# Optimization experiments

Measured on AMD Instinct MI355X. Metric: run time of the kernel, lower is better.

The kernel has to match this reference:

```python
import jax, jax.numpy as jnp
import numpy as np

EPS = 1e-6
NUM_HEADS = 12


def ln_cf(x, w, b):
    # channels_first LayerNorm over channel dim (ConvNeXt style)
    u = jnp.mean(x, axis=1, keepdims=True)
    s = jnp.mean((x - u) ** 2, axis=1, keepdims=True)
    xn = (x - u) / jnp.sqrt(s + EPS)
    shp = (1, -1) + (1,) * (x.ndim - 2)
    return xn * w.reshape(shp) + b.reshape(shp)


def conv2s2(x, w):
    # Conv3d kernel=2 stride=2 (no bias): exact non-overlapping patch contraction
    b, c, H, W, D = x.shape
    xp = x.reshape(b, c, H // 2, 2, W // 2, 2, D // 2, 2)
    return jnp.einsum('bchkwpdq,ockpq->bohwd', xp, w)


def convt2s2(x, w):
    # ConvTranspose3d kernel=2 stride=2 (torch weight layout [in, out, 2,2,2])
    b, i, H, W, D = x.shape
    o = w.shape[1]
    y = jnp.einsum('bihwd,iokpq->bohkwpdq', x, w)
    return y.reshape(b, o, 2 * H, 2 * W, 2 * D)


def stem(x, w1, g1, b1, w2, g2, b2):
    h = conv2s2(x, w1)
    h = jax.nn.gelu(ln_cf(h, g1, b1), approximate=False)
    h = conv2s2(h, w2)
    return ln_cf(h, g2, b2)


def debed(x, tw1, g, b, tw2, tb2):
    h = convt2s2(x, tw1)
    h = jax.nn.gelu(ln_cf(h, g, b), approximate=False)
    return convt2s2(h, tw2) + tb2.reshape(1, -1, 1, 1, 1)


def rope(x):
    # rotary embedding over full token dim c (pairs (i, i+c/2)), positions 0..L-1
    b, l, c = x.shape
    inv = 1.0 / (10000.0 ** (jnp.arange(0, c, 2, dtype=jnp.float32) / c))
    t = jnp.arange(l, dtype=jnp.float32)
    f = jnp.outer(t, inv)                      # [l, c/2]
    emb = jnp.concatenate([f, f], axis=-1)     # [l, c]
    cos, sin = jnp.cos(emb)[None], jnp.sin(emb)[None]
    rot = jnp.concatenate([-x[..., c // 2:], x[..., :c // 2]], axis=-1)
    return x * cos + rot * sin


def _forward(x, skip, q_w1, q_g1, q_b1, q_w2, q_g2, q_b2,
             k_w1, k_g1, k_b1, k_w2, k_g2, k_b2,
             v_w1, v_g1, v_b1, v_w2, v_g2, v_b2,
             o_tw1, o_g, o_b, o_tw2, o_tb2,
             ns_w, ns_b, nx_w, nx_b, no_w, no_b):
    res = skip
    skip = ln_cf(skip, ns_w, ns_b)
    x = ln_cf(x, nx_w, nx_b)
    q = stem(skip, q_w1, q_g1, q_b1, q_w2, q_g2, q_b2)
    k = stem(x, k_w1, k_g1, k_b1, k_w2, k_g2, k_b2)
    v = stem(x, v_w1, v_g1, v_b1, v_w2, v_g2, v_b2)
    b, c, Hq, Wq, Dq = q.shape
    _, _, Hk, Wk, Dk = k.shape
    q = q.reshape(b, c, -1).transpose(0, 2, 1)   # [b, Lq, c]
    k = k.reshape(b, c, -1).transpose(0, 2, 1)   # [b, Lk, c]
    v = v.reshape(b, c, -1).transpose(0, 2, 1)
    q = rope(q)
    k = rope(k)
    hd = c // NUM_HEADS
    qh = q.reshape(b, -1, NUM_HEADS, hd).transpose(0, 2, 1, 3)  # [b, nh, Lq, hd]
    kh = k.reshape(b, -1, NUM_HEADS, hd).transpose(0, 2, 1, 3)
    vh = v.reshape(b, -1, NUM_HEADS, hd).transpose(0, 2, 1, 3)
    scale = 1.0 / jnp.sqrt(jnp.float32(hd))
    attn = jax.nn.softmax(jnp.einsum('bhqc,bhkc->bhqk', qh, kh) * scale, axis=-1)
    proj = jnp.einsum('bhqk,bhkc->bhqc', attn, vh)              # [b, nh, Lq, hd]
    # rearrange 'b nh l c -> b (c nh) h w d'
    proj = proj.transpose(0, 3, 1, 2).reshape(b, c, Hq, Wq, Dq)
    proj = ln_cf(proj, no_w, no_b)
    out = debed(proj, o_tw1, o_g, o_b, o_tw2, o_tb2)
    return out + res


def setup_inputs() -> dict:
    key = jax.random.key(0)
    ks = iter(jax.random.split(key, 40))
    def nrm(shape, scale):
        return jax.random.normal(next(ks), shape, jnp.float32) * scale
    E, E4, XF, SF = 768, 192, 6, 6
    inp = {
        'x': nrm((2, XF, 48, 48, 48), 1.0),
        'skip': nrm((2, SF, 48, 48, 48), 1.0),
    }
    for p, ic in [('q', SF), ('k', XF), ('v', XF)]:
        inp[p + '_w1'] = nrm((E4, ic, 2, 2, 2), (ic * 8) ** -0.5)
        inp[p + '_g1'] = jnp.ones(E4, jnp.float32)
        inp[p + '_b1'] = jnp.zeros(E4, jnp.float32)
        inp[p + '_w2'] = nrm((E, E4, 2, 2, 2), (E4 * 8) ** -0.5)
        inp[p + '_g2'] = jnp.ones(E, jnp.float32)
        inp[p + '_b2'] = jnp.zeros(E, jnp.float32)
    inp['o_tw1'] = nrm((E, E4, 2, 2, 2), E ** -0.5)
    inp['o_g'] = jnp.ones(E4, jnp.float32)
    inp['o_b'] = jnp.zeros(E4, jnp.float32)
    inp['o_tw2'] = nrm((E4, SF, 2, 2, 2), E4 ** -0.5)
    inp['o_tb2'] = jnp.zeros(SF, jnp.float32)
    inp['ns_w'] = jnp.ones(SF, jnp.float32)
    inp['ns_b'] = jnp.zeros(SF, jnp.float32)
    inp['nx_w'] = jnp.ones(XF, jnp.float32)
    inp['nx_b'] = jnp.zeros(XF, jnp.float32)
    inp['no_w'] = jnp.ones(E, jnp.float32)
    inp['no_b'] = jnp.zeros(E, jnp.float32)
    return inp


def reference(x, skip, q_w1, q_g1, q_b1, q_w2, q_g2, q_b2,
              k_w1, k_g1, k_b1, k_w2, k_g2, k_b2,
              v_w1, v_g1, v_b1, v_w2, v_g2, v_b2,
              o_tw1, o_g, o_b, o_tw2, o_tb2,
              ns_w, ns_b, nx_w, nx_b, no_w, no_b):
    return _forward(x, skip, q_w1, q_g1, q_b1, q_w2, q_g2, q_b2,
                    k_w1, k_g1, k_b1, k_w2, k_g2, k_b2,
                    v_w1, v_g1, v_b1, v_w2, v_g2, v_b2,
                    o_tw1, o_g, o_b, o_tw2, o_tb2,
                    ns_w, ns_b, nx_w, nx_b, no_w, no_b)
```

## Files before the change

kernel.cpp:

```cpp
#include <hip/hip_runtime.h>
#include <math.h>

#define BB_ 2
#define C0 6
#define S0 48
#define V0 (S0*S0*S0)
#define C1 192
#define S1 24
#define V1 (S1*S1*S1)
#define C2 768
#define S2 12
#define LL (S2*S2*S2)
#define NH 12
#define HD 64
#define KDIM (C1*8)
#define MDIM (BB_*LL)

typedef __attribute__((ext_vector_type(8))) short short8;
typedef __attribute__((ext_vector_type(4))) short short4v;
typedef __attribute__((ext_vector_type(4))) float float4v;

static __device__ __forceinline__ float gelu_exact(float x){
  return 0.5f*x*(1.0f+erff(x*0.70710678118654752440f));
}
static __device__ __forceinline__ unsigned short f2bf(float f){
  unsigned int u = __float_as_uint(f);
  unsigned int r = (u + 0x7fffu + ((u>>16)&1u)) >> 16;
  return (unsigned short)r;
}
static __device__ __forceinline__ unsigned int pk_bf16(float a, float b){
#if __has_builtin(__builtin_amdgcn_cvt_pk_bf16_f32)
  typedef __attribute__((ext_vector_type(2))) __bf16 bf2;
  bf2 r = __builtin_amdgcn_cvt_pk_bf16_f32(a,b);
  union { bf2 v; unsigned int u; } cv; cv.v = r;
  return cv.u;
#else
  return (unsigned int)f2bf(a) | ((unsigned int)f2bf(b)<<16);
#endif
}
static __device__ __forceinline__ float bf2f(unsigned short u){
  return __uint_as_float(((unsigned int)u)<<16);
}
static __device__ __forceinline__ float exp2v(float x){
#if __has_builtin(__builtin_amdgcn_exp2f)
  return __builtin_amdgcn_exp2f(x);
#else
  return exp2f(x);
#endif
}
static __device__ __forceinline__ void load_lds16(const void* g, void* l){
  __builtin_amdgcn_global_load_lds((const __attribute__((address_space(1))) unsigned int*)g,
      (__attribute__((address_space(3))) unsigned int*)l, 16, 0, 0);
}
static __device__ __forceinline__ float4v mfma32(short8 a, short8 b, float4v c){
  return __builtin_amdgcn_mfma_f32_16x16x32_bf16(a,b,c,0,0,0);
}
static __device__ __forceinline__ float4v mfma16(short4v a, short4v b, float4v c){
#if __has_builtin(__builtin_amdgcn_mfma_f32_16x16x16bf16_1k)
  return __builtin_amdgcn_mfma_f32_16x16x16bf16_1k(a,b,c,0,0,0);
#else
  asm volatile("v_mfma_f32_16x16x16_bf16 %0, %1, %2, %0" : "+v"(c) : "v"(a), "v"(b));
  return c;
#endif
}

__global__ __launch_bounds__(256) void prep_kernel(
    const float* __restrict__ skin, const float* __restrict__ xin,
    const float* __restrict__ nsw, const float* __restrict__ nsb,
    const float* __restrict__ nxw, const float* __restrict__ nxb,
    unsigned short* __restrict__ outS, unsigned short* __restrict__ outX,
    const float* __restrict__ qw2, const float* __restrict__ kw2, const float* __restrict__ vw2,
    const float* __restrict__ tw1, const float* __restrict__ tw2,
    const float* __restrict__ qw1, const float* __restrict__ kw1, const float* __restrict__ vw1,
    unsigned short* __restrict__ w2tq, unsigned short* __restrict__ w2tk,
    unsigned short* __restrict__ w2tv, unsigned short* __restrict__ Btd,
    unsigned short* __restrict__ Bt48,
    unsigned short* __restrict__ w1q, unsigned short* __restrict__ w1k,
    unsigned short* __restrict__ w1v){
  int bx = blockIdx.x;
  if (bx < 1728){
    int z = bx >= 864;
    const float* in = z ? xin : skin;
    const float* w  = z ? nxw : nsw;
    const float* bi = z ? nxb : nsb;
    unsigned short* out = z ? outX : outS;
    int idx = (bx - z*864)*256 + threadIdx.x;
    int b = idx / V0, vox = idx - b*V0;
    const float* p = in + (size_t)b*(C0*V0) + vox;
    float v[C0]; float s=0.f;
#pragma unroll
    for (int c=0;c<C0;c++){ v[c]=p[(size_t)c*V0]; s+=v[c]; }
    float u = s*(1.f/C0);
    float ss=0.f;
#pragma unroll
    for (int c=0;c<C0;c++){ float d=v[c]-u; ss+=d*d; }
    float inv = rsqrtf(ss*(1.f/C0)+1e-6f);
    unsigned short* o = out + (size_t)b*(C0*V0) + vox;
#pragma unroll
    for (int c=0;c<C0;c++) o[(size_t)c*V0] = f2bf((v[c]-u)*inv*w[c]+bi[c]);
    return;
  }
  bx -= 1728;
  if (bx < 13824){
    int z = bx/4608;
    int idx = (bx - z*4608)*256 + threadIdx.x;
    const float* w2 = (z==0)?qw2:((z==1)?kw2:vw2);
    unsigned short* o = (z==0)?w2tq:((z==1)?w2tk:w2tv);
    int oc = idx/KDIM; int r = idx-oc*KDIM; int p = r/C1; int ic = r-p*C1;
    o[idx] = f2bf(w2[(size_t)oc*KDIM + ic*8 + p]);
  } else if (bx < 18432){
    int idx = (bx-13824)*256 + threadIdx.x;
    int n = idx/C2; int p = idx-n*C2;
    int i = ((p&63)*NH) + (p>>6);
    int kpq = n/C1, o2 = n-kpq*C1;
    Btd[idx] = f2bf(tw1[(size_t)i*KDIM + o2*8 + kpq]);
  } else if (bx < 18480){
    int idx = (bx-18432)*256 + threadIdx.x;
    int n = idx/C1; int i = idx-n*C1;
    Bt48[idx] = (n<48) ? f2bf(tw2[(size_t)i*48 + n]) : (unsigned short)0;
  } else {
    int idx = (bx-18480)*256 + threadIdx.x;
    int z = idx / 9216; int r = idx - z*9216;
    const float* w1 = (z==0)?qw1:((z==1)?kw1:vw1);
    unsigned short* o = (z==0)?w1q:((z==1)?w1k:w1v);
    o[r] = f2bf(w1[r]);
  }
}

__global__ __launch_bounds__(256) void conv1_kernel(
    const unsigned short* __restrict__ lnSb, const unsigned short* __restrict__ lnXb,
    const unsigned short* __restrict__ w1bq, const unsigned short* __restrict__ w1bk,
    const unsigned short* __restrict__ w1bv,
    const float* __restrict__ qg1, const float* __restrict__ qb1,
    const float* __restrict__ kg1, const float* __restrict__ kb1,
    const float* __restrict__ vg1, const float* __restrict__ vb1,
    unsigned short* __restrict__ h1q, unsigned short* __restrict__ h1k,
    unsigned short* __restrict__ h1v){
  int z = blockIdx.z;
  const unsigned short* in = (z==0)? lnSb : lnXb;
  const unsigned short* Wb = (z==0)?w1bq:((z==1)?w1bk:w1bv);
  const float* g1 = (z==0)?qg1:((z==1)?kg1:vg1);
  const float* b1 = (z==0)?qb1:((z==1)?kb1:vb1);
  unsigned short* h1p = (z==0)?h1q:((z==1)?h1k:h1v);
  int t = threadIdx.x, w = t>>6, lane = t&63;
  int g = lane>>4, l16 = lane&15;
  int j = blockIdx.x*4 + w;
  int bxh = j/18, mt = j - bxh*18;
  int b = bxh/48; int rem = bxh - b*48; int y = rem>>1, xh = rem&1;
  int xo = mt/3, zo = mt - xo*3;
  int xv = xh*12 + xo*2 + (l16>>3);
  int zv = zo*8 + (l16&7);
  int x2 = 2*xv, z2 = 2*zv, y2 = 2*y;
  const unsigned short* base = in + (size_t)b*C0*V0;
  union { short8 v; unsigned int u[4]; } aA;
  {
    size_t rb = (size_t)g*V0;
    aA.u[0] = *(const unsigned int*)&base[rb + (y2+0)*(S0*S0) + (x2+0)*S0 + z2];
    aA.u[1] = *(const unsigned int*)&base[rb + (y2+0)*(S0*S0) + (x2+1)*S0 + z2];
    aA.u[2] = *(const unsigned int*)&base[rb + (y2+1)*(S0*S0) + (x2+0)*S0 + z2];
    aA.u[3] = *(const unsigned int*)&base[rb + (y2+1)*(S0*S0) + (x2+1)*S0 + z2];
  }
  union { short4v v; unsigned int u[2]; } aB;
  {
    size_t rb = (size_t)(4+(g>>1))*V0 + (y2+(g&1))*(S0*S0);
    aB.u[0] = *(const unsigned int*)&base[rb + (x2+0)*S0 + z2];
    aB.u[1] = *(const unsigned int*)&base[rb + (x2+1)*S0 + z2];
  }
  float4v acc[12];
#pragma unroll
  for (int ot=0; ot<12; ot++){
    short8  wA = *(const short8*)&Wb[(ot*16+l16)*48 + g*8];
    short4v wB = *(const short4v*)&Wb[(ot*16+l16)*48 + 32 + g*4];
    float4v a = {};
    a = mfma32(wA, aA.v, a);
    a = mfma16(wB, aB.v, a);
    acc[ot] = a;
  }
  float s1=0.f, s2=0.f;
#pragma unroll
  for (int ot=0;ot<12;ot++)
#pragma unroll
    for (int reg=0;reg<4;reg++){ float v=acc[ot][reg]; s1+=v; s2+=v*v; }
  s1 += __shfl_xor(s1,16); s1 += __shfl_xor(s1,32);
  s2 += __shfl_xor(s2,16); s2 += __shfl_xor(s2,32);
  float u = s1*(1.f/C1);
  float inv = rsqrtf(s2*(1.f/C1)-u*u+1e-6f);
  int tok = (y>>1)*(S2*S2) + (xv>>1)*S2 + (zv>>1);
  int p8 = (y&1)*4 + (xv&1)*2 + (zv&1);
  unsigned short* hb = h1p + (size_t)(b*LL+tok)*KDIM + p8*C1;
#pragma unroll
  for (int ot=0; ot<12; ot++){
    int oc0 = ot*16 + g*4;
    float4 gg = *(const float4*)&g1[oc0];
    float4 bb = *(const float4*)&b1[oc0];
    float x0 = gelu_exact((acc[ot][0]-u)*inv*gg.x+bb.x);
    float x1 = gelu_exact((acc[ot][1]-u)*inv*gg.y+bb.y);
    float x2e= gelu_exact((acc[ot][2]-u)*inv*gg.z+bb.z);
    float x3 = gelu_exact((acc[ot][3]-u)*inv*gg.w+bb.w);
    uint2 pk; pk.x = pk_bf16(x0,x1); pk.y = pk_bf16(x2e,x3);
    *(uint2*)&hb[oc0] = pk;
  }
}

__global__ __launch_bounds__(256) void gemm_stem_kernel(
    const unsigned short* __restrict__ A0, const unsigned short* __restrict__ A1,
    const unsigned short* __restrict__ A2,
    const unsigned short* __restrict__ B0, const unsigned short* __restrict__ B1,
    const unsigned short* __restrict__ B2,
    unsigned short* __restrict__ Cq, unsigned short* __restrict__ Ck,
    unsigned short* __restrict__ Cv){
  int flat = blockIdx.x;
  int xcd = flat & 7, slot = flat >> 3;
  int tile = xcd*122 + slot;
  if (tile >= 972) return;
  int z = tile/324; int rr = tile - z*324;
  int m0 = (rr/12)*128, n0 = (rr - (rr/12)*12)*64;
  const unsigned short* A = (z==0)?A0:((z==1)?A1:A2);
  const unsigned short* Bt = (z==0)?B0:((z==1)?B1:B2);
  unsigned short* Cp = (z==0)?Cq:((z==1)?Ck:Cv);
  __shared__ __align__(16) unsigned short Al[3][128*32];
  __shared__ __align__(16) unsigned short Bl[3][64*32];
  int t=threadIdx.x, w=t>>6, lane=t&63;
  int g=lane>>4, l16=lane&15, r16=lane>>2, c16=lane&3;
  int wm=w>>1, wn=w&1;
  int csrc = (c16 ^ ((r16>>1)&3))*8;
  int crd  = (g   ^ ((l16>>1)&3))*8;
  float4v acc[4][2] = {};
  auto STAGE = [&](int buf, int kcol){
#pragma unroll
    for (int cc=0;cc<3;cc++){
      int ch = w*3+cc;
      if (ch<8) load_lds16(A + (size_t)(m0+ch*16+r16)*KDIM + kcol + csrc, &Al[buf][ch*512]);
      else      load_lds16(Bt + (size_t)(n0+(ch-8)*16+r16)*KDIM + kcol + csrc, &Bl[buf][(ch-8)*512]);
    }
  };
  auto COMPUTE = [&](int buf){
    short8 af[4], bf[2];
#pragma unroll
    for (int mt=0;mt<4;mt++) af[mt] = *(const short8*)&Al[buf][(wm*64+mt*16+l16)*32 + crd];
#pragma unroll
    for (int nt=0;nt<2;nt++) bf[nt] = *(const short8*)&Bl[buf][(wn*32+nt*16+l16)*32 + crd];
#pragma unroll
    for (int mt=0;mt<4;mt++)
#pragma unroll
      for (int nt=0;nt<2;nt++)
        acc[mt][nt] = mfma32(af[mt], bf[nt], acc[mt][nt]);
  };
  const int NT = KDIM/32;
  STAGE(0, 0);
  STAGE(1, 32);
  asm volatile("s_waitcnt vmcnt(3)" ::: "memory");
  __builtin_amdgcn_s_barrier();
  __builtin_amdgcn_sched_barrier(0);
  int cur = 0;
  for (int tt=0; tt<NT-2; tt++){
    int nb = cur+2; if (nb>=3) nb-=3;
    STAGE(nb, tt*32+64);
    COMPUTE(cur);
    __builtin_amdgcn_sched_barrier(0);
    asm volatile("s_waitcnt vmcnt(3)" ::: "memory");
    __builtin_amdgcn_s_barrier();
    __builtin_amdgcn_sched_barrier(0);
    cur++; if (cur>=3) cur-=3;
  }
  COMPUTE(cur);
  __builtin_amdgcn_sched_barrier(0);
  asm volatile("s_waitcnt vmcnt(0)" ::: "memory");
  __builtin_amdgcn_s_barrier();
  __builtin_amdgcn_sched_barrier(0);
  cur++; if (cur>=3) cur-=3;
  COMPUTE(cur);
#pragma unroll
  for (int mt=0;mt<4;mt++){
    int mb = m0 + wm*64 + mt*16 + g*4;
#pragma unroll
    for (int nt=0;nt<2;nt++){
      int col = n0 + wn*32 + nt*16 + l16;
#pragma unroll
      for (int reg=0;reg<4;reg++)
        Cp[(size_t)(mb+reg)*C2 + col] = f2bf(acc[mt][nt][reg]);
    }
  }
}

__global__ __launch_bounds__(256) void gemm_debed_kernel(const unsigned short* __restrict__ A,
    const unsigned short* __restrict__ Bt, unsigned short* __restrict__ C){
  int flat = blockIdx.x;
  int xcd = flat & 7, slot = flat >> 3;
  int tile = xcd*81 + slot;
  int m0 = (tile/24)*128, n0 = (tile - (tile/24)*24)*64;
  __shared__ __align__(16) unsigned short Al[3][128*32];
  __shared__ __align__(16) unsigned short Bl[3][64*32];
  int t=threadIdx.x, w=t>>6, lane=t&63;
  int g=lane>>4, l16=lane&15, r16=lane>>2, c16=lane&3;
  int wm=w>>1, wn=w&1;
  int csrc = (c16 ^ ((r16>>1)&3))*8;
  int crd  = (g   ^ ((l16>>1)&3))*8;
  float4v acc[4][2] = {};
  auto STAGE = [&](int buf, int kcol){
#pragma unroll
    for (int cc=0;cc<3;cc++){
      int ch = w*3+cc;
      if (ch<8) load_lds16(A + (size_t)(m0+ch*16+r16)*C2 + kcol + csrc, &Al[buf][ch*512]);
      else      load_lds16(Bt + (size_t)(n0+(ch-8)*16+r16)*C2 + kcol + csrc, &Bl[buf][(ch-8)*512]);
    }
  };
  auto COMPUTE = [&](int buf){
    short8 af[4], bf[2];
#pragma unroll
    for (int mt=0;mt<4;mt++) af[mt] = *(const short8*)&Al[buf][(wm*64+mt*16+l16)*32 + crd];
#pragma unroll
    for (int nt=0;nt<2;nt++) bf[nt] = *(const short8*)&Bl[buf][(wn*32+nt*16+l16)*32 + crd];
#pragma unroll
    for (int mt=0;mt<4;mt++)
#pragma unroll
      for (int nt=0;nt<2;nt++)
        acc[mt][nt] = mfma32(af[mt], bf[nt], acc[mt][nt]);
  };
  const int NT = C2/32;
  STAGE(0, 0);
  STAGE(1, 32);
  asm volatile("s_waitcnt vmcnt(3)" ::: "memory");
  __builtin_amdgcn_s_barrier();
  __builtin_amdgcn_sched_barrier(0);
  int cur = 0;
  for (int tt=0; tt<NT-2; tt++){
    int nb = cur+2; if (nb>=3) nb-=3;
    STAGE(nb, tt*32+64);
    COMPUTE(cur);
    __builtin_amdgcn_sched_barrier(0);
    asm volatile("s_waitcnt vmcnt(3)" ::: "memory");
    __builtin_amdgcn_s_barrier();
    __builtin_amdgcn_sched_barrier(0);
    cur++; if (cur>=3) cur-=3;
  }
  COMPUTE(cur);
  __builtin_amdgcn_sched_barrier(0);
  asm volatile("s_waitcnt vmcnt(0)" ::: "memory");
  __builtin_amdgcn_s_barrier();
  __builtin_amdgcn_sched_barrier(0);
  cur++; if (cur>=3) cur-=3;
  COMPUTE(cur);
#pragma unroll
  for (int nt=0;nt<2;nt++){
    int n = n0 + wn*32 + nt*16 + l16;
    int kpq = n / C1;
    int o = n - kpq*C1;
#pragma unroll
    for (int mt=0;mt<4;mt++){
      int mb = m0 + wm*64 + mt*16 + g*4;
#pragma unroll
      for (int reg=0;reg<4;reg++){
        int m = mb + reg;
        int b = m / LL; int tok = m - b*LL;
        int h = tok/(S2*S2), ww=(tok/S2)%S2, d=tok%S2;
        int v24 = (2*h+((kpq>>2)&1))*(S1*S1) + (2*ww+((kpq>>1)&1))*S1 + (2*d+(kpq&1));
        C[(size_t)(b*V1+v24)*C1 + o] = f2bf(acc[mt][nt][reg]);
      }
    }
  }
}

__global__ __launch_bounds__(256) void final_kernel(const unsigned short* __restrict__ dh,
    const unsigned short* __restrict__ Bt48, const float* __restrict__ og,
    const float* __restrict__ ob, const float* __restrict__ tb2s,
    const float* __restrict__ skipp, float* __restrict__ out){
  __shared__ __align__(16) unsigned short As[64*200];
  __shared__ __align__(16) unsigned short Bs[64*200];
  int t=threadIdx.x, w=t>>6, lane=t&63;
  int g=lane>>4, l16=lane&15;
  int m0 = blockIdx.x*64;
  for (int n8 = t; n8 < 1536; n8 += 256){
    int n64 = n8/24, kk = (n8 - n64*24)*8;
    uint4 d4 = *(const uint4*)&Bt48[n64*192 + kk];
    *(uint4*)&Bs[n64*200 + kk] = d4;
  }
  float g0=og[lane], g1v=og[lane+64], g2v=og[lane+128];
  float b0=ob[lane], b1v=ob[lane+64], b2v=ob[lane+128];
  for (int rr=0; rr<16; rr++){
    int rl = w*16 + rr;
    const unsigned short* row = dh + (size_t)(m0+rl)*C1;
    float v0=bf2f(row[lane]), v1=bf2f(row[lane+64]), v2=bf2f(row[lane+128]);
    float s1=v0+v1+v2, s2=v0*v0+v1*v1+v2*v2;
#pragma unroll
    for (int off=32;off>0;off>>=1){ s1+=__shfl_xor(s1,off); s2+=__shfl_xor(s2,off); }
    float u=s1*(1.f/C1), inv=rsqrtf(s2*(1.f/C1)-u*u+1e-6f);
    As[rl*200+lane]     = f2bf(gelu_exact((v0-u)*inv*g0+b0));
    As[rl*200+lane+64]  = f2bf(gelu_exact((v1-u)*inv*g1v+b1v));
    As[rl*200+lane+128] = f2bf(gelu_exact((v2-u)*inv*g2v+b2v));
  }
  __syncthreads();
  int wm=w>>1, wn=w&1;
  float4v acc[2][2] = {};
#pragma unroll
  for (int kb=0;kb<192;kb+=32){
    short8 af[2], bf[2];
#pragma unroll
    for (int mt=0;mt<2;mt++) af[mt] = *(const short8*)&As[(wm*32+mt*16+l16)*200 + kb + g*8];
#pragma unroll
    for (int nt=0;nt<2;nt++) bf[nt] = *(const short8*)&Bs[(wn*32+nt*16+l16)*200 + kb + g*8];
#pragma unroll
    for (int mt=0;mt<2;mt++)
#pragma unroll
      for (int nt=0;nt<2;nt++)
        acc[mt][nt] = mfma32(af[mt], bf[nt], acc[mt][nt]);
  }
#pragma unroll
  for (int nt=0;nt<2;nt++){
    int n = wn*32 + nt*16 + l16;
    if (n < 48){
      int c = n>>3, kpq = n&7;
      float bias = tb2s[c];
#pragma unroll
      for (int mt=0;mt<2;mt++){
        int mb = m0 + wm*32 + mt*16 + g*4;
#pragma unroll
        for (int reg=0;reg<4;reg++){
          int m = mb + reg;
          int b = m / V1; int v24 = m - b*V1;
          int y24 = v24/(S1*S1), x24=(v24/S1)%S1, z24=v24%S1;
          int vox = (2*y24+((kpq>>2)&1))*(S0*S0) + (2*x24+((kpq>>1)&1))*S0 + 2*z24+(kpq&1);
          size_t oi = (size_t)(b*C0+c)*V0 + vox;
          out[oi] = acc[mt][nt][reg] + bias + skipp[oi];
        }
      }
    }
  }
}

__global__ __launch_bounds__(256) void ln768_stem_kernel(
    unsigned short* __restrict__ qb, unsigned short* __restrict__ kb2,
    unsigned short* __restrict__ vb,
    const float* __restrict__ qg, const float* __restrict__ qbi,
    const float* __restrict__ kg, const float* __restrict__ kbi,
    const float* __restrict__ vg, const float* __restrict__ vbi, float qscale){
  int z = blockIdx.y;
  unsigned short* buf = (z==0)?qb:((z==1)?kb2:vb);
  const float* g  = (z==0)?qg:((z==1)?kg:vg);
  const float* bia= (z==0)?qbi:((z==1)?kbi:vbi);
  float scale = (z==0)? qscale : 1.0f;
  int tok = blockIdx.x*4 + (threadIdx.x>>6), lane = threadIdx.x&63;
  unsigned short* row = buf + (size_t)tok*C2;
  float v[12]; float s1=0.f,s2=0.f;
#pragma unroll
  for (int i=0;i<12;i++){ float t=bf2f(row[i*64+lane]); v[i]=t; s1+=t; s2+=t*t; }
#pragma unroll
  for (int off=32;off>0;off>>=1){ s1+=__shfl_xor(s1,off); s2+=__shfl_xor(s2,off); }
  float u=s1*(1.f/C2);
  float inv=rsqrtf(s2*(1.f/C2)-u*u+1e-6f);
  if (z==2){
#pragma unroll
    for (int i=0;i<12;i++){ int j=i*64+lane; row[j]=f2bf((v[i]-u)*inv*g[j]+bia[j]); }
  } else {
    int pos = tok % LL;
#pragma unroll
    for (int i=0;i<6;i++){
      int j=i*64+lane;
      float xn1=(v[i]-u)*inv*g[j]+bia[j];
      float xn2=(v[i+6]-u)*inv*g[j+384]+bia[j+384];
      float fr=(float)pos*__expf(-0.02398526139f*(float)j);
      float cs=cosf(fr), sn=sinf(fr);
      row[j]     = f2bf((xn1*cs - xn2*sn)*scale);
      row[j+384] = f2bf((xn2*cs + xn1*sn)*scale);
    }
  }
}

__global__ __launch_bounds__(256) void vtrans_kernel(const unsigned short* __restrict__ vbf,
    unsigned short* __restrict__ vT){
  __shared__ unsigned short T[64*72];
  int tok0 = blockIdx.x*64;
  int h = blockIdx.y, b = blockIdx.z;
  int t = threadIdx.x;
#pragma unroll
  for (int i=0;i<2;i++){
    int idx = t + i*256;
    int token = idx>>3, dc = idx&7;
    uint4 d4 = *(const uint4*)&vbf[(size_t)(b*LL+tok0+token)*C2 + h*64 + dc*8];
    const unsigned short* s = (const unsigned short*)&d4;
#pragma unroll
    for (int j2=0;j2<8;j2++) T[(dc*8+j2)*72 + token] = s[j2];
  }
  __syncthreads();
  int r = t>>2, seg = t&3;
  unsigned short* dst = vT + (size_t)((b*NH+h)*HD + r)*LL + tok0 + seg*16;
  uint4 o[2];
  unsigned short* os = (unsigned short*)o;
#pragma unroll
  for (int j2=0;j2<16;j2++) os[j2] = T[r*72 + seg*16 + j2];
  *(uint4*)dst = o[0];
  *(uint4*)(dst+8) = o[1];
}

__global__ __launch_bounds__(256) void attn_kernel(const unsigned short* __restrict__ q,
    const unsigned short* __restrict__ k, const unsigned short* __restrict__ vt,
    unsigned short* __restrict__ opart, float* __restrict__ lbuf){
  __shared__ __align__(16) unsigned char smem[32768];
  unsigned short* Ks = (unsigned short*)smem;
  unsigned short* Vs = Ks + 4096;
  int flat = blockIdx.x;
  int xcd = flat & 7, slot = flat >> 3;
  int tile = xcd*108 + slot;
  int h = tile / 72; int rem = tile - h*72;
  int zb = rem / 9, qt = rem - zb*9;
  int b = zb >> 2, split = zb & 3;
  int t=threadIdx.x, w=t>>6, lane=t&63;
  int g=lane>>4, l16=lane&15;
  short8 qA[3], qB[3];
#pragma unroll
  for (int j=0;j<3;j++){
    const unsigned short* qrow = q + (size_t)(b*LL + qt*192 + w*48 + j*16 + l16)*C2 + h*64;
    qA[j] = *(const short8*)(qrow + g*8);
    qB[j] = *(const short8*)(qrow + 32 + g*8);
  }
  const unsigned short* kbase = k + (size_t)(b*LL)*C2 + h*64;
  const unsigned short* vbase = vt + (size_t)((b*NH+h)*HD)*LL;
  int sub = lane>>3;
  int chs = (lane&7) ^ sub;
  int ktb = split*7, kte = (split==3)? 27 : (split*7+7);
  const unsigned short* gptr[4];
  unsigned short* ldst[4];
  int gstep[4];
#pragma unroll
  for (int cc=0;cc<4;cc++){
    int ii = w*4+cc;
    if (ii<8){
      int key = ktb*64 + ii*8 + sub;
      gptr[cc] = kbase + (size_t)key*C2 + chs*8;
      gstep[cc] = 64*C2;
      ldst[cc] = &Ks[ii*512];
    } else {
      int d = (ii-8)*8 + sub;
      gptr[cc] = vbase + (size_t)d*LL + ktb*64 + chs*8;
      gstep[cc] = 64;
      ldst[cc] = &Vs[(ii-8)*512];
    }
  }
  int sw = l16 & 7;
  const unsigned short* ksrow = &Ks[l16*64 + (g^sw)*8];
  int c2d = (((4+g)^sw) - (g^sw))*8;
  const unsigned short* vsrow = &Vs[l16*64 + (g&1)*4];
  int xk[4];
#pragma unroll
  for (int kc=0;kc<4;kc++) xk[kc] = (((kc*2 + (g>>1)) ^ sw))*8;
  short4v vones;
  vones[0]=vones[1]=vones[2]=vones[3]=(short)0x3F80;
  float4v O4[3][4] = {};
  float4v Ol[3] = {};
#pragma unroll
  for (int cc=0;cc<4;cc++){
    load_lds16(gptr[cc], ldst[cc]);
    gptr[cc] += gstep[cc];
  }
  __syncthreads();
  int cur = 0;
  for (int kt=ktb; kt<kte; kt++){
    if (kt+1 < kte){
      int so = (cur^1)*8192;
#pragma unroll
      for (int cc=0;cc<4;cc++){
        load_lds16(gptr[cc], ldst[cc]+so);
        gptr[cc] += gstep[cc];
      }
    }
    int co = cur*8192;
    const unsigned short* kr = ksrow + co;
    const unsigned short* vr = vsrow + co;
    float4v sc[3][4];
#pragma unroll
    for (int nt=0;nt<4;nt++){
      short8 k1 = *(const short8*)(kr + nt*1024);
      short8 k2 = *(const short8*)(kr + nt*1024 + c2d);
#pragma unroll
      for (int j=0;j<3;j++){
        float4v zz = {};
        zz = mfma32(k1, qA[j], zz);
        zz = mfma32(k2, qB[j], zz);
        sc[j][nt] = zz;
      }
    }
#pragma unroll
    for (int j=0;j<3;j++)
#pragma unroll
      for (int nt=0;nt<4;nt++)
#pragma unroll
        for (int reg=0;reg<4;reg++)
          sc[j][nt][reg] = exp2v(sc[j][nt][reg]);
    short4v pbs[3][4];
#pragma unroll
    for (int j=0;j<3;j++)
#pragma unroll
      for (int kc=0;kc<4;kc++){
        union { short4v v; unsigned int u[2]; } pb;
        pb.u[0] = pk_bf16(sc[j][kc][0], sc[j][kc][1]);
        pb.u[1] = pk_bf16(sc[j][kc][2], sc[j][kc][3]);
        pbs[j][kc] = pb.v;
      }
#pragma unroll
    for (int kc=0;kc<4;kc++){
      const unsigned short* vp = vr + xk[kc];
      short4v va[4];
#pragma unroll
      for (int dt=0;dt<4;dt++) va[dt] = *(const short4v*)(vp + dt*1024);
#pragma unroll
      for (int j=0;j<3;j++){
        Ol[j] = mfma16(vones, pbs[j][kc], Ol[j]);
#pragma unroll
        for (int dt=0;dt<4;dt++)
          O4[j][dt] = mfma16(va[dt], pbs[j][kc], O4[j][dt]);
      }
    }
    __syncthreads();
    cur ^= 1;
  }
  float* Ot = (float*)smem;
  float* ot = Ot + w*1216;
  int qq = lane>>2, c4 = lane&3;
#pragma unroll
  for (int j=0;j<3;j++){
#pragma unroll
    for (int dt=0;dt<4;dt++)
      *(float4*)&ot[l16*76 + dt*16 + g*4] =
          make_float4(O4[j][dt][0],O4[j][dt][1],O4[j][dt][2],O4[j][dt][3]);
    if (g==0){
      int qi = qt*192 + w*48 + j*16 + l16;
      lbuf[((size_t)(b*4+split)*NH+h)*LL + qi] = Ol[j][0];
    }
    unsigned short* orow = opart + (size_t)split*MDIM*C2
                + (size_t)(b*LL + qt*192 + w*48 + j*16 + qq)*C2 + h*64;
#pragma unroll
    for (int p=0;p<4;p++){
      float4 vv = *(float4*)&ot[qq*76 + p*16 + c4*4];
      uint2 pk; pk.x = pk_bf16(vv.x,vv.y); pk.y = pk_bf16(vv.z,vv.w);
      *(uint2*)&orow[p*16 + c4*4] = pk;
    }
    __syncthreads();
  }
}

__global__ __launch_bounds__(256) void attn_post_kernel(const unsigned short* __restrict__ opart,
    const float* __restrict__ lbuf,
    const float* __restrict__ g, const float* __restrict__ bia,
    unsigned short* __restrict__ aob){
  int t=threadIdx.x, w=t>>6, lane=t&63;
  int m = blockIdx.x*4 + w;
  int b = m / LL, l = m - b*LL;
  const unsigned short* o0 = opart + (size_t)m*C2;
  unsigned short* orow = aob + (size_t)m*C2;
  float vv[12]; float s1=0.f, s2=0.f;
#pragma unroll
  for (int i=0;i<12;i++){
    float ls = 0.f;
#pragma unroll
    for (int s=0;s<4;s++) ls += lbuf[((size_t)(b*4+s)*NH+i)*LL + l];
    float inv = 1.f/ls;
    int j = i*64+lane;
    float val = 0.f;
#pragma unroll
    for (int s=0;s<4;s++) val += bf2f(o0[(size_t)s*MDIM*C2 + j]);
    val *= inv;
    vv[i]=val; s1+=val; s2+=val*val;
  }
#pragma unroll
  for (int off=32;off>0;off>>=1){ s1+=__shfl_xor(s1,off); s2+=__shfl_xor(s2,off); }
  float u=s1*(1.f/C2);
  float invs=rsqrtf(s2*(1.f/C2)-u*u+1e-6f);
#pragma unroll
  for (int i=0;i<12;i++){
    int cj = lane*NH + i;
    orow[i*64+lane] = f2bf((vv[i]-u)*invs*g[cj]+bia[cj]);
  }
}

extern "C" void kernel_launch(void* const* d_in, const int* in_sizes, int n_in,
                              void* d_out, int out_size, void* d_ws, size_t ws_size,
                              hipStream_t stream){
  (void)in_sizes; (void)n_in; (void)out_size; (void)ws_size;
  const float* x    =(const float*)d_in[0];
  const float* skip =(const float*)d_in[1];
  const float* q_w1 =(const float*)d_in[2];
  const float* q_g1 =(const float*)d_in[3];
  const float* q_b1 =(const float*)d_in[4];
  const float* q_w2 =(const float*)d_in[5];
  const float* q_g2 =(const float*)d_in[6];
  const float* q_b2 =(const float*)d_in[7];
  const float* k_w1 =(const float*)d_in[8];
  const float* k_g1 =(const float*)d_in[9];
  const float* k_b1 =(const float*)d_in[10];
  const float* k_w2 =(const float*)d_in[11];
  const float* k_g2 =(const float*)d_in[12];
  const float* k_b2 =(const float*)d_in[13];
  const float* v_w1 =(const float*)d_in[14];
  const float* v_g1 =(const float*)d_in[15];
  const float* v_b1 =(const float*)d_in[16];
  const float* v_w2 =(const float*)d_in[17];
  const float* v_g2 =(const float*)d_in[18];
  const float* v_b2 =(const float*)d_in[19];
  const float* o_tw1=(const float*)d_in[20];
  const float* o_g  =(const float*)d_in[21];
  const float* o_b  =(const float*)d_in[22];
  const float* o_tw2=(const float*)d_in[23];
  const float* o_tb2=(const float*)d_in[24];
  const float* ns_w =(const float*)d_in[25];
  const float* ns_b =(const float*)d_in[26];
  const float* nx_w =(const float*)d_in[27];
  const float* nx_b =(const float*)d_in[28];
  const float* no_w =(const float*)d_in[29];
  const float* no_b =(const float*)d_in[30];
  float* out=(float*)d_out;

  char* W = (char*)d_ws;
  unsigned short* lnSb = (unsigned short*)(W + 0);
  unsigned short* lnXb = (unsigned short*)(W + 2654208);
  unsigned short* h1q  = (unsigned short*)(W + 5308416);
  unsigned short* h1k  = (unsigned short*)(W + 15925248);
  unsigned short* h1v  = (unsigned short*)(W + 26542080);
  unsigned short* w2tq = (unsigned short*)(W + 37158912);
  unsigned short* w2tk = (unsigned short*)(W + 39518208);
  unsigned short* w2tv = (unsigned short*)(W + 41877504);
  unsigned short* qbf  = (unsigned short*)(W + 44236800);
  unsigned short* kbf  = (unsigned short*)(W + 49545216);
  unsigned short* vbf  = (unsigned short*)(W + 54853632);
  unsigned short* vT   = (unsigned short*)(W + 60162048);
  unsigned short* aob  = (unsigned short*)(W + 65470464);
  unsigned short* Btd  = (unsigned short*)(W + 70778880);
  unsigned short* Bt48 = (unsigned short*)(W + 73138176);
  unsigned short* w1q  = (unsigned short*)(W + 73162752);
  unsigned short* w1k  = (unsigned short*)(W + 73181184);
  unsigned short* w1v  = (unsigned short*)(W + 73199616);
  float* lbuf  = (float*)(W + 0);
  unsigned short* opart = (unsigned short*)(W + 5308416);
  unsigned short* dh   = (unsigned short*)(W + 5308416);

  const float QSCALE = 0.125f*1.44269504089f;

  prep_kernel<<<20316,256,0,stream>>>(skip, x, ns_w, ns_b, nx_w, nx_b, lnSb, lnXb,
      q_w2,k_w2,v_w2,o_tw1,o_tw2, q_w1,k_w1,v_w1,
      w2tq,w2tk,w2tv,Btd,Bt48, w1q,w1k,w1v);
  conv1_kernel<<<dim3(432,1,3),256,0,stream>>>(lnSb,lnXb, w1q,w1k,w1v,
      q_g1,q_b1, k_g1,k_b1, v_g1,v_b1, h1q,h1k,h1v);
  gemm_stem_kernel<<<976,256,0,stream>>>(h1q,h1k,h1v,
      w2tq,w2tk,w2tv, qbf,kbf,vbf);
  ln768_stem_kernel<<<dim3(864,3),256,0,stream>>>(qbf,kbf,vbf,
      q_g2,q_b2, k_g2,k_b2, v_g2,v_b2, QSCALE);
  vtrans_kernel<<<dim3(27,12,2),256,0,stream>>>(vbf, vT);
  attn_kernel<<<864,256,0,stream>>>(qbf, kbf, vT, opart, lbuf);
  attn_post_kernel<<<864,256,0,stream>>>(opart, lbuf, no_w, no_b, aob);
  gemm_debed_kernel<<<648,256,0,stream>>>(aob, Btd, dh);
  final_kernel<<<432,256,0,stream>>>(dh, Bt48, o_g, o_b, o_tb2, skip, out);
}
```

Measured before the change: 324.9 us.

## Pre-tile GEMM operands into contiguous K-blocks for streaming LDS loads

The producers (prep weight transposes, conv1 output, attention post-norm output) now write A and B operands in a blocked layout: each 128-row (or 64-row) by 32-column K tile is stored as one contiguous chunk. The two GEMM kernels then stream these chunks with a precomputed, pointer-incremented global_load_lds address instead of strided row addressing. This is meant to make each stage fetch contiguous memory and cut per-iteration address arithmetic. It also drops a sched_barrier after COMPUTE. The cost is scattered writes in the producers and a layout coupling across several kernels.

```diff
diff --git a/kernel.cpp b/kernel.cpp
--- a/kernel.cpp
+++ b/kernel.cpp
@@ -63,6 +63,7 @@
   return c;
 #endif
 }
+
 
 __global__ __launch_bounds__(256) void prep_kernel(
     const float* __restrict__ skin, const float* __restrict__ xin,
@@ -106,14 +107,16 @@
     int idx = (bx - z*4608)*256 + threadIdx.x;
     const float* w2 = (z==0)?qw2:((z==1)?kw2:vw2);
     unsigned short* o = (z==0)?w2tq:((z==1)?w2tk:w2tv);
-    int oc = idx/KDIM; int r = idx-oc*KDIM; int p = r/C1; int ic = r-p*C1;
-    o[idx] = f2bf(w2[(size_t)oc*KDIM + ic*8 + p]);
+    int oc = idx/KDIM; int k = idx-oc*KDIM; int p = k/C1; int ic = k-p*C1;
+    size_t dst = ((size_t)(oc>>6)*48 + (k>>5))*2048 + (oc&63)*32 + (k&31);
+    o[dst] = f2bf(w2[(size_t)oc*KDIM + ic*8 + p]);
   } else if (bx < 18432){
     int idx = (bx-13824)*256 + threadIdx.x;
     int n = idx/C2; int p = idx-n*C2;
     int i = ((p&63)*NH) + (p>>6);
     int kpq = n/C1, o2 = n-kpq*C1;
-    Btd[idx] = f2bf(tw1[(size_t)i*KDIM + o2*8 + kpq]);
+    size_t dst = ((size_t)(n>>6)*24 + (p>>5))*2048 + (n&63)*32 + (p&31);
+    Btd[dst] = f2bf(tw1[(size_t)i*KDIM + o2*8 + kpq]);
   } else if (bx < 18480){
     int idx = (bx-18432)*256 + threadIdx.x;
     int n = idx/C1; int i = idx-n*C1;
@@ -187,7 +190,8 @@
   float inv = rsqrtf(s2*(1.f/C1)-u*u+1e-6f);
   int tok = (y>>1)*(S2*S2) + (xv>>1)*S2 + (zv>>1);
   int p8 = (y&1)*4 + (xv&1)*2 + (zv&1);
-  unsigned short* hb = h1p + (size_t)(b*LL+tok)*KDIM + p8*C1;
+  int m_ = b*LL + tok;
+  unsigned short* hb = h1p + ((size_t)(m_>>7)*48)*4096 + (size_t)(m_&127)*32;
 #pragma unroll
   for (int ot=0; ot<12; ot++){
     int oc0 = ot*16 + g*4;
@@ -198,7 +202,8 @@
     float x2e= gelu_exact((acc[ot][2]-u)*inv*gg.z+bb.z);
     float x3 = gelu_exact((acc[ot][3]-u)*inv*gg.w+bb.w);
     uint2 pk; pk.x = pk_bf16(x0,x1); pk.y = pk_bf16(x2e,x3);
-    *(uint2*)&hb[oc0] = pk;
+    int kblk = p8*6 + (oc0>>5);
+    *(uint2*)&hb[(size_t)kblk*4096 + (oc0&31)] = pk;
   }
 }
 
@@ -214,26 +219,39 @@
   int tile = xcd*122 + slot;
   if (tile >= 972) return;
   int z = tile/324; int rr = tile - z*324;
-  int m0 = (rr/12)*128, n0 = (rr - (rr/12)*12)*64;
+  int mp = rr/12, np = rr - mp*12;
   const unsigned short* A = (z==0)?A0:((z==1)?A1:A2);
   const unsigned short* Bt = (z==0)?B0:((z==1)?B1:B2);
   unsigned short* Cp = (z==0)?Cq:((z==1)?Ck:Cv);
-  __shared__ __align__(16) unsigned short Al[3][128*32];
-  __shared__ __align__(16) unsigned short Bl[3][64*32];
+  __shared__ __align__(16) unsigned short Al[3][4096];
+  __shared__ __align__(16) unsigned short Bl[3][2048];
   int t=threadIdx.x, w=t>>6, lane=t&63;
-  int g=lane>>4, l16=lane&15, r16=lane>>2, c16=lane&3;
+  int g=lane>>4, l16=lane&15;
   int wm=w>>1, wn=w&1;
-  int csrc = (c16 ^ ((r16>>1)&3))*8;
-  int crd  = (g   ^ ((l16>>1)&3))*8;
+  int loff = (lane>>2)*32 + (((lane&3) ^ ((lane>>3)&3))<<3);
+  int crd  = (g ^ ((l16>>1)&3))*8;
+  const unsigned short* gp[3];
+  unsigned short* ld[3];
+  int step[3];
+#pragma unroll
+  for (int cc=0;cc<3;cc++){
+    int ch = w*3+cc;
+    if (ch<8){
+      gp[cc] = A + ((size_t)mp*48)*4096 + ch*512 + loff;
+      step[cc] = 4096; ld[cc] = &Al[0][ch*512];
+    } else {
+      gp[cc] = Bt + ((size_t)np*48)*2048 + (ch-8)*512 + loff;
+      step[cc] = 2048; ld[cc] = &Bl[0][(ch-8)*512];
+    }
+  }
+  auto STAGE = [&](int buf){
+#pragma unroll
+    for (int cc=0;cc<3;cc++){
+      load_lds16(gp[cc], ld[cc] + buf*step[cc]);
+      gp[cc] += step[cc];
+    }
+  };
   float4v acc[4][2] = {};
-  auto STAGE = [&](int buf, int kcol){
-#pragma unroll
-    for (int cc=0;cc<3;cc++){
-      int ch = w*3+cc;
-      if (ch<8) load_lds16(A + (size_t)(m0+ch*16+r16)*KDIM + kcol + csrc, &Al[buf][ch*512]);
-      else      load_lds16(Bt + (size_t)(n0+(ch-8)*16+r16)*KDIM + kcol + csrc, &Bl[buf][(ch-8)*512]);
-    }
-  };
   auto COMPUTE = [&](int buf){
     short8 af[4], bf[2];
 #pragma unroll
@@ -246,30 +264,28 @@
       for (int nt=0;nt<2;nt++)
         acc[mt][nt] = mfma32(af[mt], bf[nt], acc[mt][nt]);
   };
-  const int NT = KDIM/32;
-  STAGE(0, 0);
-  STAGE(1, 32);
+  const int NT = 48;
+  STAGE(0); STAGE(1);
   asm volatile("s_waitcnt vmcnt(3)" ::: "memory");
   __builtin_amdgcn_s_barrier();
   __builtin_amdgcn_sched_barrier(0);
   int cur = 0;
   for (int tt=0; tt<NT-2; tt++){
     int nb = cur+2; if (nb>=3) nb-=3;
-    STAGE(nb, tt*32+64);
+    STAGE(nb);
     COMPUTE(cur);
-    __builtin_amdgcn_sched_barrier(0);
     asm volatile("s_waitcnt vmcnt(3)" ::: "memory");
     __builtin_amdgcn_s_barrier();
     __builtin_amdgcn_sched_barrier(0);
     cur++; if (cur>=3) cur-=3;
   }
   COMPUTE(cur);
-  __builtin_amdgcn_sched_barrier(0);
   asm volatile("s_waitcnt vmcnt(0)" ::: "memory");
   __builtin_amdgcn_s_barrier();
   __builtin_amdgcn_sched_barrier(0);
   cur++; if (cur>=3) cur-=3;
   COMPUTE(cur);
+  int m0 = mp*128, n0 = np*64;
 #pragma unroll
   for (int mt=0;mt<4;mt++){
     int mb = m0 + wm*64 + mt*16 + g*4;
@@ -288,23 +304,36 @@
   int flat = blockIdx.x;
   int xcd = flat & 7, slot = flat >> 3;
   int tile = xcd*81 + slot;
-  int m0 = (tile/24)*128, n0 = (tile - (tile/24)*24)*64;
-  __shared__ __align__(16) unsigned short Al[3][128*32];
-  __shared__ __align__(16) unsigned short Bl[3][64*32];
+  int mp = tile/24, np = tile - mp*24;
+  __shared__ __align__(16) unsigned short Al[3][4096];
+  __shared__ __align__(16) unsigned short Bl[3][2048];
   int t=threadIdx.x, w=t>>6, lane=t&63;
-  int g=lane>>4, l16=lane&15, r16=lane>>2, c16=lane&3;
+  int g=lane>>4, l16=lane&15;
   int wm=w>>1, wn=w&1;
-  int csrc = (c16 ^ ((r16>>1)&3))*8;
-  int crd  = (g   ^ ((l16>>1)&3))*8;
+  int loff = (lane>>2)*32 + (((lane&3) ^ ((lane>>3)&3))<<3);
+  int crd  = (g ^ ((l16>>1)&3))*8;
+  const unsigned short* gp[3];
+  unsigned short* ld[3];
+  int step[3];
+#pragma unroll
+  for (int cc=0;cc<3;cc++){
+    int ch = w*3+cc;
+    if (ch<8){
+      gp[cc] = A + ((size_t)mp*24)*4096 + ch*512 + loff;
+      step[cc] = 4096; ld[cc] = &Al[0][ch*512];
+    } else {
+      gp[cc] = Bt + ((size_t)np*24)*2048 + (ch-8)*512 + loff;
+      step[cc] = 2048; ld[cc] = &Bl[0][(ch-8)*512];
+    }
+  }
+  auto STAGE = [&](int buf){
+#pragma unroll
+    for (int cc=0;cc<3;cc++){
+      load_lds16(gp[cc], ld[cc] + buf*step[cc]);
+      gp[cc] += step[cc];
+    }
+  };
   float4v acc[4][2] = {};
-  auto STAGE = [&](int buf, int kcol){
-#pragma unroll
-    for (int cc=0;cc<3;cc++){
-      int ch = w*3+cc;
-      if (ch<8) load_lds16(A + (size_t)(m0+ch*16+r16)*C2 + kcol + csrc, &Al[buf][ch*512]);
-      else      load_lds16(Bt + (size_t)(n0+(ch-8)*16+r16)*C2 + kcol + csrc, &Bl[buf][(ch-8)*512]);
-    }
-  };
   auto COMPUTE = [&](int buf){
     short8 af[4], bf[2];
 #pragma unroll
@@ -317,30 +346,28 @@
       for (int nt=0;nt<2;nt++)
         acc[mt][nt] = mfma32(af[mt], bf[nt], acc[mt][nt]);
   };
-  const int NT = C2/32;
-  STAGE(0, 0);
-  STAGE(1, 32);
+  const int NT = 24;
+  STAGE(0); STAGE(1);
   asm volatile("s_waitcnt vmcnt(3)" ::: "memory");
   __builtin_amdgcn_s_barrier();
   __builtin_amdgcn_sched_barrier(0);
   int cur = 0;
   for (int tt=0; tt<NT-2; tt++){
     int nb = cur+2; if (nb>=3) nb-=3;
-    STAGE(nb, tt*32+64);
+    STAGE(nb);
     COMPUTE(cur);
-    __builtin_amdgcn_sched_barrier(0);
     asm volatile("s_waitcnt vmcnt(3)" ::: "memory");
     __builtin_amdgcn_s_barrier();
     __builtin_amdgcn_sched_barrier(0);
     cur++; if (cur>=3) cur-=3;
   }
   COMPUTE(cur);
-  __builtin_amdgcn_sched_barrier(0);
   asm volatile("s_waitcnt vmcnt(0)" ::: "memory");
   __builtin_amdgcn_s_barrier();
   __builtin_amdgcn_sched_barrier(0);
   cur++; if (cur>=3) cur-=3;
   COMPUTE(cur);
+  int m0 = mp*128, n0 = np*64;
 #pragma unroll
   for (int nt=0;nt<2;nt++){
     int n = n0 + wn*32 + nt*16 + l16;
@@ -646,7 +673,8 @@
   int m = blockIdx.x*4 + w;
   int b = m / LL, l = m - b*LL;
   const unsigned short* o0 = opart + (size_t)m*C2;
-  unsigned short* orow = aob + (size_t)m*C2;
+  unsigned short* ob2 = aob + ((size_t)(m>>7)*24)*4096 + (size_t)(m&127)*32
+                        + (lane&31) + (size_t)(lane>>5)*4096;
   float vv[12]; float s1=0.f, s2=0.f;
 #pragma unroll
   for (int i=0;i<12;i++){
@@ -668,7 +696,7 @@
 #pragma unroll
   for (int i=0;i<12;i++){
     int cj = lane*NH + i;
-    orow[i*64+lane] = f2bf((vv[i]-u)*invs*g[cj]+bia[cj]);
+    ob2[(size_t)i*8192] = f2bf((vv[i]-u)*invs*g[cj]+bia[cj]);
   }
 }
 
```

Measured after the change: 308.9 us. 4.9% less time.
